# Performance work log

Measured on AMD Instinct MI355X. Metric: run time of the kernel, lower is better.

The kernel has to match this reference:

```python
import jax, jax.numpy as jnp
import numpy as np

TOP_K = 8
NORM_TOPK_PROB = False


def setup_inputs() -> dict:
    key = jax.random.key(0)
    k1, k2 = jax.random.split(key)
    hidden_states = jax.random.normal(k1, (4, 8192, 2048), dtype=jnp.float32)
    # gate weight: [n_experts=64, hidden_dim=2048], like nn.Linear weight
    weight = jax.random.normal(k2, (64, 2048), dtype=jnp.float32) * 0.02
    return {"hidden_states": hidden_states, "weight": weight}


def reference(hidden_states, weight):
    hidden_dim = weight.shape[1]
    x = hidden_states.reshape(-1, hidden_dim)            # [N, D]
    router_logits = jnp.einsum('nd,ed->ne', x, weight)   # [N, E] F.linear
    # softmax in float32 (dtype=torch.float), returned as the "logits"
    router_probs = jax.nn.softmax(router_logits.astype(jnp.float32), axis=-1)
    router_top_value, router_indices = jax.lax.top_k(router_probs, TOP_K)
    if NORM_TOPK_PROB:
        router_top_value = router_top_value / jnp.sum(router_top_value, axis=-1, keepdims=True)
    router_top_value = router_top_value.astype(router_probs.dtype)
    return (router_probs, router_top_value, router_indices)
```

## Files before the change

### kernel.cpp

```cpp
#include <hip/hip_runtime.h>
#include <math.h>


constexpr int HD = 2048, NE = 64, RPB = 64, BK = 64, NT = HD / BK, TOPK = 8;
constexpr float XSC = 4096.f;
constexpr float WSC = 8192.f;
constexpr float DESCALE = 1.0f / (XSC * WSC);

typedef _Float16 f16x8 __attribute__((ext_vector_type(8)));
typedef float f32x4 __attribute__((ext_vector_type(4)));
typedef void __attribute__((address_space(1)))* gas_t;
typedef void __attribute__((address_space(3)))* las_t;

__device__ __forceinline__ void gload_lds16(const void* g, void* l) {
  __builtin_amdgcn_global_load_lds((gas_t)(uintptr_t)g, (las_t)l, 16, 0, 0);
}

__global__ __launch_bounds__(256)
void wprep_k(const float* __restrict__ W, char* __restrict__ WP) {
  const int b = blockIdx.x;
  const int t = threadIdx.x;
  const int nt = t >> 6, q = (t >> 4) & 3, m = t & 15;
  const float* src = W + (size_t)(nt * 16 + m) * HD + b * 32 + q * 8;
  f16x8 hi, lo;
#pragma unroll
  for (int j = 0; j < 8; ++j) {
    float a = src[j] * WSC;
    _Float16 ha = (_Float16)a;
    hi[j] = ha;
    lo[j] = (_Float16)(a - (float)ha);
  }
  char* dst = WP + ((size_t)b * 8 + nt * 2) * 1024 + (q * 16 + m) * 16;
  *(f16x8*)dst = hi;
  *(f16x8*)(dst + 1024) = lo;
}

__global__ __launch_bounds__(256, 2)
void router_k(const float* __restrict__ X, const char* __restrict__ WP,
              float* __restrict__ probs, float* __restrict__ topv,
              float* __restrict__ topi) {
  __shared__ float4 smem4[5120];
  char* smem = (char*)smem4;

  const int tid = threadIdx.x, wv = tid >> 6, lane = tid & 63;
  const int m_l = lane & 15, q_l = lane >> 4;
  const int rowbase = blockIdx.x * RPB;

  const int kq_st = m_l ^ ((4 * wv + q_l) & 15);
  const float* gx = X + (size_t)(rowbase + 4 * wv + q_l) * HD + kq_st * 4;
  const char* gw = WP + lane * 16;

  f32x4 acc_hh[4], acc_cr[4];
#pragma unroll
  for (int nt = 0; nt < 4; ++nt) {
    acc_hh[nt] = {0.f, 0.f, 0.f, 0.f};
    acc_cr[nt] = {0.f, 0.f, 0.f, 0.f};
  }

#pragma unroll
  for (int j = 0; j < 4; ++j)
    gload_lds16(gw + (4 * wv + j) * 1024, smem + 49152 + (4 * wv + j) * 1024);
  __builtin_amdgcn_sched_barrier(0);
#pragma unroll
  for (int m = 0; m < 4; ++m)
    gload_lds16(gx + (size_t)m * 16 * HD, smem + (4 * m + wv) * 1024);
  __builtin_amdgcn_sched_barrier(0);
#pragma unroll
  for (int m = 0; m < 4; ++m)
    gload_lds16(gx + (size_t)m * 16 * HD + BK, smem + 16384 + (4 * m + wv) * 1024);
  __builtin_amdgcn_sched_barrier(0);

  int xc = 0, xn = 2;
  for (int t = 0; t < NT; ++t) {
    if (t == NT - 1) {
      asm volatile("s_waitcnt vmcnt(0)" ::: "memory");
    } else {
      asm volatile("s_waitcnt vmcnt(4)" ::: "memory");
    }
    __builtin_amdgcn_s_barrier();
    __builtin_amdgcn_sched_barrier(0);

    if (t + 1 < NT) {
      char* wd = smem + 49152 + ((t + 1) & 1) * 16384;
      const char* ws = gw + (size_t)(t + 1) * 16384;
#pragma unroll
      for (int j = 0; j < 4; ++j)
        gload_lds16(ws + (4 * wv + j) * 1024, wd + (4 * wv + j) * 1024);
    }
    __builtin_amdgcn_sched_barrier(0);
    if (t + 2 < NT) {
      char* xd = smem + xn * 16384;
#pragma unroll
      for (int m = 0; m < 4; ++m)
        gload_lds16(gx + (size_t)m * 16 * HD + (t + 2) * BK, xd + (4 * m + wv) * 1024);
    }
    __builtin_amdgcn_sched_barrier(0);

    char* xcur = smem + xc * 16384;
    char* wcur = smem + 49152 + (t & 1) * 16384;
#pragma unroll
    for (int s = 0; s < 2; ++s) {
      const int row_l = 16 * wv + m_l;
      const int kq0 = 8 * s + 2 * q_l;
      const int G0 = row_l * 16 + (kq0 ^ m_l);
      const int G1 = row_l * 16 + ((kq0 + 1) ^ m_l);
      f32x4 xa = *(const f32x4*)(xcur + G0 * 16);
      f32x4 xb = *(const f32x4*)(xcur + G1 * 16);
      f16x8 ah, al;
#pragma unroll
      for (int j = 0; j < 4; ++j) {
        float a = xa[j] * XSC; _Float16 ha = (_Float16)a;
        ah[j] = ha; al[j] = (_Float16)(a - (float)ha);
        float b = xb[j] * XSC; _Float16 hb = (_Float16)b;
        ah[j + 4] = hb; al[j + 4] = (_Float16)(b - (float)hb);
      }
#pragma unroll
      for (int nt = 0; nt < 4; ++nt) {
        f16x8 bh = *(const f16x8*)(wcur + (s * 8 + nt * 2) * 1024 + lane * 16);
        f16x8 bl = *(const f16x8*)(wcur + (s * 8 + nt * 2 + 1) * 1024 + lane * 16);
        acc_hh[nt] = __builtin_amdgcn_mfma_f32_16x16x32_f16(ah, bh, acc_hh[nt], 0, 0, 0);
        acc_cr[nt] = __builtin_amdgcn_mfma_f32_16x16x32_f16(ah, bl, acc_cr[nt], 0, 0, 0);
        acc_cr[nt] = __builtin_amdgcn_mfma_f32_16x16x32_f16(al, bh, acc_cr[nt], 0, 0, 0);
      }
    }
    xc = (xc + 1 < 3) ? xc + 1 : 0;
    xn = (xn + 1 < 3) ? xn + 1 : 0;
  }

  __syncthreads();
  float* plds = (float*)smem;
#pragma unroll
  for (int nt = 0; nt < 4; ++nt)
#pragma unroll
    for (int r = 0; r < 4; ++r)
      plds[(16 * wv + 4 * q_l + r) * 68 + nt * 16 + m_l] =
          (acc_hh[nt][r] + acc_cr[nt][r]) * DESCALE;
  __syncthreads();

  for (int rr = 0; rr < 16; ++rr) {
    const int row_l = wv * 16 + rr;
    const float lg = plds[row_l * 68 + lane];

    float mx = lg;
#pragma unroll
    for (int off = 32; off; off >>= 1)
      mx = fmaxf(mx, __shfl_xor(mx, off, 64));

    const float ex = expf(lg - mx);
    float sm = ex;
#pragma unroll
    for (int off = 32; off; off >>= 1)
      sm += __shfl_xor(sm, off, 64);

    const float p = ex * (1.0f / sm);
    probs[(size_t)(rowbase + row_l) * NE + lane] = p;

    int rank = 0;
#pragma unroll
    for (int j = 0; j < NE; ++j) {
      const float pj = __shfl(p, j, 64);
      rank += (pj > p) || (pj == p && j < lane);
    }
    if (rank < TOPK) {
      topv[(size_t)(rowbase + row_l) * TOPK + rank] = p;
      topi[(size_t)(rowbase + row_l) * TOPK + rank] = (float)lane;
    }
  }
}

extern "C" void kernel_launch(void* const* d_in, const int* in_sizes, int n_in,
                              void* d_out, int out_size, void* d_ws, size_t ws_size,
                              hipStream_t stream) {
  const float* X = (const float*)d_in[0];
  const float* W = (const float*)d_in[1];
  const int n = in_sizes[0] / HD;

  float* probs = (float*)d_out;
  float* topv  = probs + (size_t)n * NE;
  float* topi  = topv + (size_t)n * TOPK;
  char* WP = (char*)d_ws;

  hipLaunchKernelGGL(wprep_k, dim3(64), dim3(256), 0, stream, W, WP);
  hipLaunchKernelGGL(router_k, dim3(n / RPB), dim3(256), 0, stream,
                     X, WP, probs, topv, topi);
}
```

Before: 425.8 us.

## Split K across waves with register-resident weights and LDS cross-wave reduction

Replaces the LDS-staged, M-split pipeline with a K-split scheme. Each of 8 waves keeps its slice of the split-fp16 weights in registers and streams X rows straight from global memory into registers. Partial logits are reduced across waves through an LDS stage buffer into a 128-row accumulator. The aim is to remove LDS traffic and async-copy bookkeeping for X and W and to reuse weights from registers. The cost is heavy register pressure (32 f16x8 weight fragments), two block barriers per 16-row chunk, and no explicit prefetch depth beyond one chunk.

```diff
diff --git a/kernel.cpp b/kernel.cpp
--- a/kernel.cpp
+++ b/kernel.cpp
@@ -2,19 +2,13 @@
 #include <math.h>
 
 
-constexpr int HD = 2048, NE = 64, RPB = 64, BK = 64, NT = HD / BK, TOPK = 8;
+constexpr int HD = 2048, NE = 64, TOPK = 8;
 constexpr float XSC = 4096.f;
 constexpr float WSC = 8192.f;
 constexpr float DESCALE = 1.0f / (XSC * WSC);
 
 typedef _Float16 f16x8 __attribute__((ext_vector_type(8)));
 typedef float f32x4 __attribute__((ext_vector_type(4)));
-typedef void __attribute__((address_space(1)))* gas_t;
-typedef void __attribute__((address_space(3)))* las_t;
-
-__device__ __forceinline__ void gload_lds16(const void* g, void* l) {
-  __builtin_amdgcn_global_load_lds((gas_t)(uintptr_t)g, (las_t)l, 16, 0, 0);
-}
 
 __global__ __launch_bounds__(256)
 void wprep_k(const float* __restrict__ W, char* __restrict__ WP) {
@@ -35,111 +29,94 @@
   *(f16x8*)(dst + 1024) = lo;
 }
 
-__global__ __launch_bounds__(256, 2)
+__global__ __launch_bounds__(512, 2)
 void router_k(const float* __restrict__ X, const char* __restrict__ WP,
               float* __restrict__ probs, float* __restrict__ topv,
               float* __restrict__ topi) {
-  __shared__ float4 smem4[5120];
-  char* smem = (char*)smem4;
+  __shared__ float stage[8][16][68];
+  __shared__ float logacc[128][68];
 
   const int tid = threadIdx.x, wv = tid >> 6, lane = tid & 63;
-  const int m_l = lane & 15, q_l = lane >> 4;
-  const int rowbase = blockIdx.x * RPB;
+  const int m = lane & 15, q = lane >> 4;
+  const int rowbase = blockIdx.x * 128;
 
-  const int kq_st = m_l ^ ((4 * wv + q_l) & 15);
-  const float* gx = X + (size_t)(rowbase + 4 * wv + q_l) * HD + kq_st * 4;
-  const char* gw = WP + lane * 16;
+  for (int p = 0; p < 2; ++p) {
+    f16x8 bh[4][4], bl[4][4];
+#pragma unroll
+    for (int s = 0; s < 4; ++s)
+#pragma unroll
+      for (int nt = 0; nt < 4; ++nt) {
+        const char* wp =
+            WP + ((size_t)(p * 32 + wv * 4 + s) * 8 + nt * 2) * 1024 + lane * 16;
+        bh[s][nt] = *(const f16x8*)wp;
+        bl[s][nt] = *(const f16x8*)(wp + 1024);
+      }
 
-  f32x4 acc_hh[4], acc_cr[4];
+    const float* xp = X + (size_t)(rowbase + m) * HD + p * 1024 + wv * 128 + q * 8;
+
+    f32x4 xa[4], xb[4];
 #pragma unroll
-  for (int nt = 0; nt < 4; ++nt) {
-    acc_hh[nt] = {0.f, 0.f, 0.f, 0.f};
-    acc_cr[nt] = {0.f, 0.f, 0.f, 0.f};
-  }
+    for (int s = 0; s < 4; ++s) {
+      xa[s] = *(const f32x4*)(xp + s * 32);
+      xb[s] = *(const f32x4*)(xp + s * 32 + 4);
+    }
+
+    for (int c = 0; c < 8; ++c) {
+      f32x4 acc_hh[4], acc_cr[4];
+#pragma unroll
+      for (int nt = 0; nt < 4; ++nt) {
+        acc_hh[nt] = {0.f, 0.f, 0.f, 0.f};
+        acc_cr[nt] = {0.f, 0.f, 0.f, 0.f};
+      }
 
 #pragma unroll
-  for (int j = 0; j < 4; ++j)
-    gload_lds16(gw + (4 * wv + j) * 1024, smem + 49152 + (4 * wv + j) * 1024);
-  __builtin_amdgcn_sched_barrier(0);
+      for (int s = 0; s < 4; ++s) {
+        f32x4 ca = xa[s], cb = xb[s];
+        if (c + 1 < 8) {
+          xa[s] = *(const f32x4*)(xp + 16 * HD + s * 32);
+          xb[s] = *(const f32x4*)(xp + 16 * HD + s * 32 + 4);
+        }
+        f16x8 ah, al;
 #pragma unroll
-  for (int m = 0; m < 4; ++m)
-    gload_lds16(gx + (size_t)m * 16 * HD, smem + (4 * m + wv) * 1024);
-  __builtin_amdgcn_sched_barrier(0);
+        for (int j = 0; j < 4; ++j) {
+          float a = ca[j] * XSC; _Float16 ha = (_Float16)a;
+          ah[j] = ha; al[j] = (_Float16)(a - (float)ha);
+          float b = cb[j] * XSC; _Float16 hb = (_Float16)b;
+          ah[j + 4] = hb; al[j + 4] = (_Float16)(b - (float)hb);
+        }
 #pragma unroll
-  for (int m = 0; m < 4; ++m)
-    gload_lds16(gx + (size_t)m * 16 * HD + BK, smem + 16384 + (4 * m + wv) * 1024);
-  __builtin_amdgcn_sched_barrier(0);
+        for (int nt = 0; nt < 4; ++nt) {
+          acc_hh[nt] = __builtin_amdgcn_mfma_f32_16x16x32_f16(ah, bh[s][nt], acc_hh[nt], 0, 0, 0);
+          acc_cr[nt] = __builtin_amdgcn_mfma_f32_16x16x32_f16(ah, bl[s][nt], acc_cr[nt], 0, 0, 0);
+          acc_cr[nt] = __builtin_amdgcn_mfma_f32_16x16x32_f16(al, bh[s][nt], acc_cr[nt], 0, 0, 0);
+        }
+      }
+      xp += 16 * HD;
 
-  int xc = 0, xn = 2;
-  for (int t = 0; t < NT; ++t) {
-    if (t == NT - 1) {
-      asm volatile("s_waitcnt vmcnt(0)" ::: "memory");
-    } else {
-      asm volatile("s_waitcnt vmcnt(4)" ::: "memory");
+#pragma unroll
+      for (int nt = 0; nt < 4; ++nt)
+#pragma unroll
+        for (int r = 0; r < 4; ++r)
+          stage[wv][q * 4 + r][nt * 16 + m] =
+              (acc_hh[nt][r] + acc_cr[nt][r]) * DESCALE;
+      __syncthreads();
+
+#pragma unroll
+      for (int rr = 0; rr < 2; ++rr) {
+        const int r = wv * 2 + rr;
+        float v = stage[0][r][lane];
+#pragma unroll
+        for (int s = 1; s < 8; ++s) v += stage[s][r][lane];
+        if (p == 0) logacc[c * 16 + r][lane] = v;
+        else        logacc[c * 16 + r][lane] += v;
+      }
+      __syncthreads();
     }
-    __builtin_amdgcn_s_barrier();
-    __builtin_amdgcn_sched_barrier(0);
-
-    if (t + 1 < NT) {
-      char* wd = smem + 49152 + ((t + 1) & 1) * 16384;
-      const char* ws = gw + (size_t)(t + 1) * 16384;
-#pragma unroll
-      for (int j = 0; j < 4; ++j)
-        gload_lds16(ws + (4 * wv + j) * 1024, wd + (4 * wv + j) * 1024);
-    }
-    __builtin_amdgcn_sched_barrier(0);
-    if (t + 2 < NT) {
-      char* xd = smem + xn * 16384;
-#pragma unroll
-      for (int m = 0; m < 4; ++m)
-        gload_lds16(gx + (size_t)m * 16 * HD + (t + 2) * BK, xd + (4 * m + wv) * 1024);
-    }
-    __builtin_amdgcn_sched_barrier(0);
-
-    char* xcur = smem + xc * 16384;
-    char* wcur = smem + 49152 + (t & 1) * 16384;
-#pragma unroll
-    for (int s = 0; s < 2; ++s) {
-      const int row_l = 16 * wv + m_l;
-      const int kq0 = 8 * s + 2 * q_l;
-      const int G0 = row_l * 16 + (kq0 ^ m_l);
-      const int G1 = row_l * 16 + ((kq0 + 1) ^ m_l);
-      f32x4 xa = *(const f32x4*)(xcur + G0 * 16);
-      f32x4 xb = *(const f32x4*)(xcur + G1 * 16);
-      f16x8 ah, al;
-#pragma unroll
-      for (int j = 0; j < 4; ++j) {
-        float a = xa[j] * XSC; _Float16 ha = (_Float16)a;
-        ah[j] = ha; al[j] = (_Float16)(a - (float)ha);
-        float b = xb[j] * XSC; _Float16 hb = (_Float16)b;
-        ah[j + 4] = hb; al[j + 4] = (_Float16)(b - (float)hb);
-      }
-#pragma unroll
-      for (int nt = 0; nt < 4; ++nt) {
-        f16x8 bh = *(const f16x8*)(wcur + (s * 8 + nt * 2) * 1024 + lane * 16);
-        f16x8 bl = *(const f16x8*)(wcur + (s * 8 + nt * 2 + 1) * 1024 + lane * 16);
-        acc_hh[nt] = __builtin_amdgcn_mfma_f32_16x16x32_f16(ah, bh, acc_hh[nt], 0, 0, 0);
-        acc_cr[nt] = __builtin_amdgcn_mfma_f32_16x16x32_f16(ah, bl, acc_cr[nt], 0, 0, 0);
-        acc_cr[nt] = __builtin_amdgcn_mfma_f32_16x16x32_f16(al, bh, acc_cr[nt], 0, 0, 0);
-      }
-    }
-    xc = (xc + 1 < 3) ? xc + 1 : 0;
-    xn = (xn + 1 < 3) ? xn + 1 : 0;
   }
-
-  __syncthreads();
-  float* plds = (float*)smem;
-#pragma unroll
-  for (int nt = 0; nt < 4; ++nt)
-#pragma unroll
-    for (int r = 0; r < 4; ++r)
-      plds[(16 * wv + 4 * q_l + r) * 68 + nt * 16 + m_l] =
-          (acc_hh[nt][r] + acc_cr[nt][r]) * DESCALE;
-  __syncthreads();
 
   for (int rr = 0; rr < 16; ++rr) {
     const int row_l = wv * 16 + rr;
-    const float lg = plds[row_l * 68 + lane];
+    const float lg = logacc[row_l][lane];
 
     float mx = lg;
 #pragma unroll
@@ -181,6 +158,6 @@
   char* WP = (char*)d_ws;
 
   hipLaunchKernelGGL(wprep_k, dim3(64), dim3(256), 0, stream, W, WP);
-  hipLaunchKernelGGL(router_k, dim3(n / RPB), dim3(256), 0, stream,
+  hipLaunchKernelGGL(router_k, dim3(n / 128), dim3(512), 0, stream,
                      X, WP, probs, topv, topi);
 }
```

New measurement: 409.2 us. -3.9%, faster.
